# Kernel tuning notes

Hardware: AMD Instinct MI355X
Metric: run time of the kernel (lower is better)

The kernel has to match this reference:

```python
import jax, jax.numpy as jnp
import numpy as np

B, T, F = 2048, 128, 128
H, L, K = 512, 8, 10  # hidden_dim, levels, conv_size
CHUNK = H // L
GATES = 4 * H + 2 * L


def setup_inputs() -> dict:
    key = jax.random.key(0)
    ks = jax.random.split(key, 12)
    s_k = 1.0 / np.sqrt(F + 1)
    s_r = 1.0 / np.sqrt(H + 1)
    s_s = 1.0 / np.sqrt(H)
    s_rs = 1.0 / np.sqrt(H // 6)
    s_c = 1.0 / np.sqrt(H * K)
    return {
        'x': jax.random.normal(ks[0], (B, T, F), jnp.float32),
        'time': jax.random.uniform(ks[1], (B, T), jnp.float32),
        'Wk': jax.random.normal(ks[2], (F + 1, GATES), jnp.float32) * s_k,
        'bk': jnp.zeros((GATES,), jnp.float32),
        'Wr': jax.random.normal(ks[3], (H + 1, GATES), jnp.float32) * s_r,
        'br': jnp.zeros((GATES,), jnp.float32),
        'Ws': jax.random.normal(ks[4], (H, H // 6), jnp.float32) * s_s,
        'bs': jax.random.normal(ks[5], (H // 6,), jnp.float32) * 0.01,
        'Wrs': jax.random.normal(ks[6], (H // 6, H), jnp.float32) * s_rs,
        'brs': jax.random.normal(ks[7], (H,), jnp.float32) * 0.01,
        'conv_w': jax.random.normal(ks[8], (H, H, K), jnp.float32) * s_c,  # [out_ch, in_ch, k]
        'conv_b': jax.random.normal(ks[9], (H,), jnp.float32) * 0.01,
    }


def _cumax_l2r(z):
    return jnp.cumsum(jax.nn.softmax(z, axis=-1), axis=-1)


def _cumax_r2l(z):
    return jnp.flip(jnp.cumsum(jax.nn.softmax(jnp.flip(z, -1), axis=-1), axis=-1), -1)


def _phase_forward(x, time, Wk, bk, Wr, br, Ws, bs, Wrs, brs, conv_w, conv_b):
    def step(carry, xs):
        c, h, tmp_h, tmp_dis = carry
        xt, dt = xs
        dt = dt[:, None]
        xo = (jnp.concatenate([xt, dt], -1) @ Wk + bk
              + jnp.concatenate([h, dt], -1) @ Wr + br)  # [B, 4H+2L]
        fm = _cumax_l2r(xo[:, :L])[:, :, None]        # [B, L, 1]
        im = _cumax_r2l(xo[:, L:2 * L])[:, :, None]   # [B, L, 1]
        g = xo[:, 2 * L:].reshape(-1, 4 * L, CHUNK)
        f = jax.nn.sigmoid(g[:, :L])
        i = jax.nn.sigmoid(g[:, L:2 * L])
        o = jax.nn.sigmoid(g[:, 2 * L:3 * L])
        c_in = jnp.tanh(g[:, 3 * L:])
        c_last = c.reshape(-1, L, CHUNK)
        ov = fm * im
        c_new = ov * (f * c_last + i * c_in) + (fm - ov) * c_last + (im - ov) * c_in
        h_new = (o * jnp.tanh(c_new)).reshape(-1, H)
        dist = 1.0 - jnp.mean(fm[..., 0], axis=-1)   # [B]
        tmp_h = jnp.concatenate([tmp_h[1:], h_new[None]], 0)
        tmp_dis = jnp.concatenate([tmp_dis[1:], dist[None]], 0)
        return (c_new.reshape(-1, H), h_new, tmp_h, tmp_dis), dist

    init = (jnp.zeros((B, H), x.dtype), jnp.zeros((B, H), x.dtype),
            jnp.zeros((K, B, H), x.dtype), jnp.zeros((K, B), x.dtype))
    (_, _, tmp_h, tmp_dis), distance = jax.lax.scan(
        step, init, (jnp.transpose(x, (1, 0, 2)), time.T))

    local_dis = jax.nn.softmax(jnp.cumsum(tmp_dis.T, axis=1), axis=1)   # [B, K]
    local_h = jnp.transpose(tmp_h, (1, 2, 0)) * local_dis[:, None, :]   # [B, H, K]
    theme = jax.nn.sigmoid(
        jnp.maximum(jnp.mean(local_h, axis=-1) @ Ws + bs, 0.0) @ Wrs + brs)  # [B, H]
    conv_out = jnp.einsum('bhk,ohk->bo', local_h, conv_w) + conv_b      # valid conv, out len 1
    return theme * conv_out, distance


def reference(x, time, Wk, bk, Wr, br, Ws, bs, Wrs, brs, conv_w, conv_b):
    return _phase_forward(x, time, Wk, bk, Wr, br, Ws, bs, Wrs, brs, conv_w, conv_b)
```

## Files before the change

### kernel.cpp

```cpp
#include <hip/hip_runtime.h>
#include <hip/hip_bf16.h>
#include <cstddef>
#include <cstdint>

namespace {

constexpr int B = 2048, T = 128, F = 128, H = 512, L = 8, KW = 10;
constexpr int GATES = 2064;
constexpr int NG = 2048;
constexpr int KIN = 640;
constexpr int HS = 85;
constexpr int RC = H * KW;
constexpr int KS = 8;
constexpr int NROW = 144;

typedef __attribute__((ext_vector_type(8))) short short8;
typedef __attribute__((ext_vector_type(4))) float f32x4;
typedef unsigned long long ull;

__device__ __forceinline__ float fsigmoid_(float x) {
    return __builtin_amdgcn_rcpf(1.0f + __expf(-x));
}
__device__ __forceinline__ float ftanh_(float x) {
    return 1.0f - 2.0f * __builtin_amdgcn_rcpf(1.0f + __expf(2.0f * x));
}

__device__ __forceinline__ void gl_lds16(const void* g, void* l) {
    __builtin_amdgcn_global_load_lds(
        (const __attribute__((address_space(1))) unsigned int*)g,
        (__attribute__((address_space(3))) unsigned int*)l,
        16, 0, 0);
}

__device__ __forceinline__ ull h_atomic_load(const void* p) {
    return __hip_atomic_load((const ull*)p, __ATOMIC_RELAXED, __HIP_MEMORY_SCOPE_AGENT);
}

__global__ __launch_bounds__(256) void prep_wgt(
    const float* __restrict__ Wk, const float* __restrict__ Wr,
    __hip_bfloat16* __restrict__ WgT)
{
    __shared__ float tile[64 * 65];
    const int tid = threadIdx.x;
    const int c0 = blockIdx.x * 64, k0 = blockIdx.y * 64;
#pragma unroll
    for (int rep = 0; rep < 16; ++rep) {
        int e = rep * 256 + tid;
        int kl = e >> 6, cl = e & 63;
        int col = c0 + cl;
        int nt = col >> 7, cc = col & 127;
        int n = 16 + ((cc >> 4) & 3) * 512 + nt * 32 + ((cc >> 6) & 1) * 16 + (cc & 15);
        int k = k0 + kl;
        tile[kl * 65 + cl] = (k < F) ? Wk[(size_t)k * GATES + n] : Wr[(size_t)(k - F) * GATES + n];
    }
    __syncthreads();
    const int cl = tid >> 2, q = tid & 3;
    unsigned short buf[16];
#pragma unroll
    for (int i = 0; i < 16; ++i) {
        float f = tile[(q * 16 + i) * 65 + cl];
        __hip_bfloat16 bv = __float2bfloat16(f);
        buf[i] = *(unsigned short*)&bv;
    }
    int col = c0 + cl;
    int nt = col >> 7, rin = col & 127;
    unsigned short* dst = (unsigned short*)WgT + (size_t)nt * NROW * KIN + (size_t)rin * KIN + k0 + q * 16;
    *(short8*)dst = *(short8*)&buf[0];
    *(short8*)(dst + 8) = *(short8*)&buf[8];
}

__global__ void prep_w16rep(const float* __restrict__ Wk, const float* __restrict__ Wr,
                            __hip_bfloat16* __restrict__ WgT)
{
    int idx = blockIdx.x * blockDim.x + threadIdx.x;
    if (idx >= 16 * 16 * KIN) return;
    int nt = idx / (16 * KIN);
    int rem = idx % (16 * KIN);
    int n = rem / KIN, k = rem % KIN;
    float v = (k < F) ? Wk[(size_t)k * GATES + n] : Wr[(size_t)(k - F) * GATES + n];
    WgT[(size_t)nt * NROW * KIN + (size_t)(128 + n) * KIN + k] = __float2bfloat16(v);
}

__global__ void prep_small(const float* __restrict__ Wk, const float* __restrict__ bk,
                           const float* __restrict__ Wr, const float* __restrict__ br,
                           float* __restrict__ biasg, float* __restrict__ wrowg,
                           float* __restrict__ bias16, float* __restrict__ wrow16)
{
    const int total = 2 * NG + 32;
    for (int idx = threadIdx.x; idx < total; idx += 256) {
        if (idx < NG) {
            int col = idx;
            int nt = col >> 7, cc = col & 127;
            int n = 16 + ((cc >> 4) & 3) * 512 + nt * 32 + ((cc >> 6) & 1) * 16 + (cc & 15);
            biasg[col] = bk[n] + br[n];
        } else if (idx < 2 * NG) {
            int col = idx - NG;
            int nt = col >> 7, cc = col & 127;
            int n = 16 + ((cc >> 4) & 3) * 512 + nt * 32 + ((cc >> 6) & 1) * 16 + (cc & 15);
            wrowg[col] = Wk[(size_t)F * GATES + n] + Wr[(size_t)H * GATES + n];
        } else if (idx < 2 * NG + 16) {
            int n = idx - 2 * NG;
            bias16[n] = bk[n] + br[n];
        } else {
            int n = idx - 2 * NG - 16;
            wrow16[n] = Wk[(size_t)F * GATES + n] + Wr[(size_t)H * GATES + n];
        }
    }
}

__global__ void convert_x(const float* __restrict__ x, __hip_bfloat16* __restrict__ xb) {
    int i = blockIdx.x * blockDim.x + threadIdx.x;
    size_t o = (size_t)i * 4;
    if (o >= (size_t)B * T * F) return;
    float4 v = *(const float4*)(x + o);
    xb[o + 0] = __float2bfloat16(v.x);
    xb[o + 1] = __float2bfloat16(v.y);
    xb[o + 2] = __float2bfloat16(v.z);
    xb[o + 3] = __float2bfloat16(v.w);
}

__global__ void prep_convw(const float* __restrict__ conv_w, __hip_bfloat16* __restrict__ CWb) {
    int i = blockIdx.x * blockDim.x + threadIdx.x;
    if (i >= H * RC / 4) return;
    size_t o = (size_t)i * 4;
    float4 v = *(const float4*)(conv_w + o);
    CWb[o + 0] = __float2bfloat16(v.x);
    CWb[o + 1] = __float2bfloat16(v.y);
    CWb[o + 2] = __float2bfloat16(v.z);
    CWb[o + 3] = __float2bfloat16(v.w);
}

struct StepArgs {
    const __hip_bfloat16* xb;
    __hip_bfloat16* h0;
    __hip_bfloat16* h1;
    const __hip_bfloat16* WgT;
    const float* biasg;
    const float* wrowg;
    const float* bias16;
    const float* wrow16;
    const float* tme;
    __hip_bfloat16* tmp_h;
    float* tmp_ds;
    float* dist_out;
    unsigned* bar;
};

__global__ __launch_bounds__(512, 2) void persistent_step(StepArgs a)
{
    __shared__ __align__(16) char smem[34816];
    float* logitS = (float*)smem;
    float* fmimS = (float*)(smem + 8704);
    unsigned short* hstageS = (unsigned short*)(smem + 16896);
    float* dts = (float*)(smem + 25088);

    const int tid = threadIdx.x;
    const int wave = tid >> 6;
    const int wr = wave >> 1, wc = wave & 1;
    const int quad = (tid & 63) >> 4, m16 = tid & 15;
    const int l = blockIdx.x;
    const int nt = ((l & 7) << 1) | ((l >> 3) & 1);
    const int mt = l >> 4;
    const int m0 = mt * 128;

    const int o0 = tid * 16;
    const int arow = o0 >> 6;
    const int asl = ((((o0 >> 4) & 3) ^ ((arow >> 1) & 3)) << 3);
    const char* xbT = (const char*)a.xb + (size_t)(m0 + arow) * (T * F * 2) + asl * 2;
    const size_t hbyte = (size_t)(m0 + arow) * (H * 2) + asl * 2;
    const unsigned short* wgt_tile = (const unsigned short*)a.WgT + (size_t)nt * NROW * KIN;
    const int brow0 = o0 >> 6;
    const int bsl0 = ((((o0 >> 4) & 3) ^ ((brow0 >> 1) & 3)) << 3);
    const char* bsT0 = (const char*)(wgt_tile + (size_t)brow0 * KIN + bsl0);
    const int ob1 = 8192 + tid * 16;
    const int brow1 = ob1 >> 6;
    const int bsl1 = ((((ob1 >> 4) & 3) ^ ((brow1 >> 1) & 3)) << 3);
    const char* bsT1 = (const char*)(wgt_tile + (size_t)brow1 * KIN + bsl1);
    const bool bv1 = (tid < 64);

    const int hcol = nt * 32 + wc * 16 + m16;
    const int lidx = hcol >> 6;
    float bj[4], wj[4];
#pragma unroll
    for (int j = 0; j < 4; ++j) {
        int col = nt * 128 + wc * 64 + j * 16 + m16;
        bj[j] = a.biasg[col];
        wj[j] = a.wrowg[col];
    }
    float b16r[16], w16r[16];
#pragma unroll
    for (int n = 0; n < 16; ++n) { b16r[n] = a.bias16[n]; w16r[n] = a.wrow16[n]; }

    const unsigned short* Abase = (const unsigned short*)smem;
    const unsigned short* Bbase = (const unsigned short*)(smem + 16384);

    float creg[2][4] = {};
    ull areg[2][2];

    {
        gl_lds16(xbT, smem + o0);
        gl_lds16(bsT0, smem + 16384 + o0);
        if (bv1) gl_lds16(bsT1, smem + 16384 + ob1);
        areg[1][0] = *(const ull*)(xbT + 64);  areg[1][1] = *(const ull*)(xbT + 72);
        areg[0][0] = *(const ull*)(xbT + 128); areg[0][1] = *(const ull*)(xbT + 136);
    }
    __syncthreads();

#pragma unroll 1
    for (int t = 0; t < T; ++t) {
        const char* xt = xbT + (size_t)t * 256;
        const char* hs = (const char*)((t & 1) ? a.h1 : a.h0) + hbyte;
        unsigned* hout32 = (unsigned*)((t & 1) ? a.h0 : a.h1);

        f32x4 acc[2][4] = {};
        f32x4 acc16[2] = {};

#pragma unroll
        for (int ki = 0; ki < 20; ++ki) {
            if (ki > 0) {
                if (ki == 1)
                    asm volatile("s_waitcnt vmcnt(1) lgkmcnt(0)" ::: "memory");
                else if (ki <= 17)
                    asm volatile("s_waitcnt vmcnt(2) lgkmcnt(0)" ::: "memory");
                else
                    asm volatile("s_waitcnt vmcnt(0) lgkmcnt(0)" ::: "memory");
                __builtin_amdgcn_s_barrier();
                __builtin_amdgcn_sched_barrier(0);
            }
            const int nxt = ki + 1;
            if (nxt < 20) {
                char* adst = smem + (nxt & 1) * 8192 + o0;
                *(ull*)adst = areg[nxt & 1][0];
                *(ull*)(adst + 8) = areg[nxt & 1][1];
                char* bdst = smem + 16384 + (nxt & 1) * 9216;
                gl_lds16(bsT0 + nxt * 64, bdst + o0);
                if (bv1) gl_lds16(bsT1 + nxt * 64, bdst + ob1);
                __builtin_amdgcn_sched_barrier(0);
                const int fut = ki + 3;
                if (fut < 20) {
                    if (fut <= 3) {
                        areg[fut & 1][0] = *(const ull*)(xt + fut * 64);
                        areg[fut & 1][1] = *(const ull*)(xt + fut * 64 + 8);
                    } else {
                        areg[fut & 1][0] = h_atomic_load(hs + fut * 64 - 256);
                        areg[fut & 1][1] = h_atomic_load(hs + fut * 64 - 248);
                    }
                }
            }
            const unsigned short* A = Abase + (ki & 1) * 4096;
            const unsigned short* Bb = Bbase + (ki & 1) * 4608;
            short8 av[2], bv[4];
#pragma unroll
            for (int i = 0; i < 2; ++i) {
                int ar = wr * 32 + i * 16 + m16;
                av[i] = *(const short8*)&A[ar * 32 + ((quad ^ ((ar >> 1) & 3)) << 3)];
            }
#pragma unroll
            for (int j = 0; j < 4; ++j) {
                int br = wc * 64 + j * 16 + m16;
                bv[j] = *(const short8*)&Bb[br * 32 + ((quad ^ ((br >> 1) & 3)) << 3)];
            }
#pragma unroll
            for (int i = 0; i < 2; ++i)
#pragma unroll
                for (int j = 0; j < 4; ++j)
                    acc[i][j] = __builtin_amdgcn_mfma_f32_16x16x32_bf16(av[i], bv[j], acc[i][j], 0, 0, 0);
            if (wc == 0) {
                int lr = 128 + m16;
                short8 wv = *(const short8*)&Bb[lr * 32 + ((quad ^ ((lr >> 1) & 3)) << 3)];
                acc16[0] = __builtin_amdgcn_mfma_f32_16x16x32_bf16(av[0], wv, acc16[0], 0, 0, 0);
                acc16[1] = __builtin_amdgcn_mfma_f32_16x16x32_bf16(av[1], wv, acc16[1], 0, 0, 0);
            }
        }
        __syncthreads();

        if (wc == 0) {
#pragma unroll
            for (int i = 0; i < 2; ++i)
#pragma unroll
                for (int r = 0; r < 4; ++r)
                    logitS[(wr * 32 + i * 16 + quad * 4 + r) * 17 + m16] = acc16[i][r];
        }
        __syncthreads();

        if (tid < 256) {
            const int row = tid & 127;
            const int m = m0 + row;
            const bool hi = tid >= 128;
            const float dt = a.tme[(size_t)m * T + t];
            if (!hi) dts[row] = dt;
            const int off = hi ? 8 : 0;
            float z[8];
#pragma unroll
            for (int n = 0; n < 8; ++n)
                z[n] = logitS[row * 17 + off + n] + b16r[off + n] + dt * w16r[off + n];
            float mx = z[0];
#pragma unroll
            for (int j = 1; j < 8; ++j) mx = fmaxf(mx, z[j]);
            float e[8], s = 0.f;
#pragma unroll
            for (int j = 0; j < 8; ++j) { e[j] = __expf(z[j] - mx); s += e[j]; }
            if (!hi) {
                float run = 0.f, fsum = 0.f;
#pragma unroll
                for (int j = 0; j < 8; ++j) { run += e[j]; float fmv = run / s; fmimS[row * 16 + j] = fmv; fsum += fmv; }
                if (nt == 0) {
                    float d = 1.0f - fsum * 0.125f;
                    a.dist_out[(size_t)t * B + m] = d;
                    if (t >= T - KW) a.tmp_ds[(size_t)(t - (T - KW)) * B + m] = d;
                }
            } else {
                float run = 0.f;
#pragma unroll
                for (int j = 7; j >= 0; --j) { run += e[j]; fmimS[row * 16 + 8 + j] = run / s; }
            }
        }
        __syncthreads();

#pragma unroll
        for (int i = 0; i < 2; ++i) {
#pragma unroll
            for (int r = 0; r < 4; ++r) {
                int rl = wr * 32 + i * 16 + quad * 4 + r;
                int m = m0 + rl;
                float dt = dts[rl];
                float fmv = fmimS[rl * 16 + lidx];
                float imv = fmimS[rl * 16 + 8 + lidx];
                float fg = fsigmoid_(acc[i][0][r] + bj[0] + dt * wj[0]);
                float ig = fsigmoid_(acc[i][1][r] + bj[1] + dt * wj[1]);
                float og = fsigmoid_(acc[i][2][r] + bj[2] + dt * wj[2]);
                float ci = ftanh_(acc[i][3][r] + bj[3] + dt * wj[3]);
                float ov = fmv * imv;
                float cl = creg[i][r];
                float cn = ov * (fg * cl + ig * ci) + (fmv - ov) * cl + (imv - ov) * ci;
                float hn = og * ftanh_(cn);
                creg[i][r] = cn;
                __hip_bfloat16 hb = __float2bfloat16(hn);
                hstageS[rl * 32 + (wc * 16 + m16)] = *(unsigned short*)&hb;
                if (t >= T - KW) a.tmp_h[((size_t)(t - (T - KW)) * B + m) * H + hcol] = hb;
            }
        }
        __syncthreads();

        {
            const unsigned* hs32 = (const unsigned*)hstageS;
#pragma unroll
            for (int wds = 0; wds < 4; ++wds) {
                int wi = wds * 512 + tid;
                int row = wi >> 4, cp = wi & 15;
                unsigned v = hs32[row * 16 + cp];
                __hip_atomic_store(hout32 + (size_t)(m0 + row) * (H / 2) + nt * 16 + cp, v,
                                   __ATOMIC_RELAXED, __HIP_MEMORY_SCOPE_AGENT);
            }
        }

        __syncthreads();
        if (t != T - 1) {
            const char* xn = xbT + (size_t)(t + 1) * 256;
            gl_lds16(xn, smem + o0);
            gl_lds16(bsT0, smem + 16384 + o0);
            if (bv1) gl_lds16(bsT1, smem + 16384 + ob1);
            areg[1][0] = *(const ull*)(xn + 64);  areg[1][1] = *(const ull*)(xn + 72);
            areg[0][0] = *(const ull*)(xn + 128); areg[0][1] = *(const ull*)(xn + 136);
            if (tid == 0) {
                unsigned* ctr = a.bar + (mt << 6);
                __hip_atomic_fetch_add(ctr, 1u, __ATOMIC_RELAXED, __HIP_MEMORY_SCOPE_AGENT);
                const unsigned tgt = 16u * (unsigned)(t + 1);
                for (int it = 0; it < (1 << 22); ++it) {
                    if (__hip_atomic_load(ctr, __ATOMIC_RELAXED, __HIP_MEMORY_SCOPE_AGENT) >= tgt) break;
                    __builtin_amdgcn_s_sleep(2);
                }
            }
            __syncthreads();
        }
    }
}

__global__ __launch_bounds__(128) void post_local(
    const __hip_bfloat16* __restrict__ tmp_h, const float* __restrict__ tmp_dis,
    float* __restrict__ mean_h, __hip_bfloat16* __restrict__ Ahk)
{
    const int b = blockIdx.x;
    const int tid = threadIdx.x;
    __shared__ float ld[KW];
    if (tid == 0) {
        float cd[KW];
        float run = 0.f;
        for (int k = 0; k < KW; ++k) { run += tmp_dis[(size_t)k * B + b]; cd[k] = run; }
        float mx = cd[0];
        for (int k = 1; k < KW; ++k) mx = fmaxf(mx, cd[k]);
        float s = 0.f;
        for (int k = 0; k < KW; ++k) { cd[k] = expf(cd[k] - mx); s += cd[k]; }
        for (int k = 0; k < KW; ++k) ld[k] = cd[k] / s;
    }
    __syncthreads();
    float ldr[KW];
#pragma unroll
    for (int k = 0; k < KW; ++k) ldr[k] = ld[k];
    for (int h = tid; h < H; h += 128) {
        float s = 0.f;
#pragma unroll
        for (int k = 0; k < KW; ++k) {
            float v = __bfloat162float(tmp_h[((size_t)k * B + b) * H + h]) * ldr[k];
            s += v;
            Ahk[(size_t)b * RC + h * KW + k] = __float2bfloat16(v);
        }
        mean_h[(size_t)b * H + h] = s * (1.0f / KW);
    }
}

__global__ void theme1_k(const float* __restrict__ mean_h, const float* __restrict__ Ws,
                         const float* __restrict__ bs, float* __restrict__ t1)
{
    int idx = blockIdx.x * blockDim.x + threadIdx.x;
    if (idx >= B * HS) return;
    int b = idx / HS, j = idx % HS;
    float s = bs[j];
    const float* mh = mean_h + (size_t)b * H;
    for (int h = 0; h < H; ++h) s += mh[h] * Ws[(size_t)h * HS + j];
    t1[idx] = fmaxf(s, 0.f);
}

__global__ void theme2_k(const float* __restrict__ t1, const float* __restrict__ Wrs,
                         const float* __restrict__ brs, float* __restrict__ theme)
{
    int idx = blockIdx.x * blockDim.x + threadIdx.x;
    if (idx >= B * H) return;
    int b = idx / H, o = idx % H;
    float s = brs[o];
    const float* tv = t1 + (size_t)b * HS;
    for (int j = 0; j < HS; ++j) s += tv[j] * Wrs[(size_t)j * H + o];
    theme[idx] = 1.0f / (1.0f + expf(-s));
}

__global__ __launch_bounds__(256) void conv_split(
    const __hip_bfloat16* __restrict__ Ahk, const __hip_bfloat16* __restrict__ CWb,
    float* __restrict__ Pbuf)
{
    __shared__ __align__(16) unsigned short As2[128 * 64];
    __shared__ __align__(16) unsigned short Bs2[128 * 64];
    const int tid = threadIdx.x;
    const int wave = tid >> 6;
    const int wr = wave >> 1, wc = wave & 1;
    const int quad = (tid & 63) >> 4, m16 = tid & 15;
    const int n0 = blockIdx.x * 128, m0 = blockIdx.y * 128;
    const int ksb = blockIdx.z * (RC / KS);

    f32x4 acc[4][4] = {};
    for (int k0 = 0; k0 < RC / KS; k0 += 64) {
#pragma unroll
        for (int p = 0; p < 4; ++p) {
            int o = p * 4096 + tid * 16;
            int row = o >> 7, slot = (o >> 4) & 7;
            int kg = ksb + k0 + (slot ^ (row & 7)) * 8;
            gl_lds16((const unsigned short*)Ahk + (size_t)(m0 + row) * RC + kg, (char*)As2 + o);
            gl_lds16((const unsigned short*)CWb + (size_t)(n0 + row) * RC + kg, (char*)Bs2 + o);
        }
        __syncthreads();
#pragma unroll
        for (int c2 = 0; c2 < 2; ++c2) {
            const int k8 = c2 * 4 + quad;
            short8 av[4], bv[4];
#pragma unroll
            for (int i = 0; i < 4; ++i) {
                int arow = wr * 64 + i * 16 + m16;
                av[i] = *(const short8*)&As2[arow * 64 + (k8 ^ (arow & 7)) * 8];
            }
#pragma unroll
            for (int j = 0; j < 4; ++j) {
                int brow = wc * 64 + j * 16 + m16;
                bv[j] = *(const short8*)&Bs2[brow * 64 + (k8 ^ (brow & 7)) * 8];
            }
#pragma unroll
            for (int i = 0; i < 4; ++i)
#pragma unroll
                for (int j = 0; j < 4; ++j)
                    acc[i][j] = __builtin_amdgcn_mfma_f32_16x16x32_bf16(av[i], bv[j], acc[i][j], 0, 0, 0);
        }
        __syncthreads();
    }
    float* P = Pbuf + (size_t)blockIdx.z * B * H;
#pragma unroll
    for (int j = 0; j < 4; ++j) {
        const int col = n0 + wc * 64 + j * 16 + m16;
#pragma unroll
        for (int i = 0; i < 4; ++i) {
            const int rb = m0 + wr * 64 + i * 16 + quad * 4;
#pragma unroll
            for (int r = 0; r < 4; ++r)
                P[(size_t)(rb + r) * H + col] = acc[i][j][r];
        }
    }
}

__global__ void conv_reduce(const float* __restrict__ Pbuf, const float* __restrict__ conv_b,
                            const float* __restrict__ theme, float* __restrict__ out0)
{
    int i = blockIdx.x * blockDim.x + threadIdx.x;
    if (i >= B * H) return;
    float s = conv_b[i & (H - 1)];
#pragma unroll
    for (int ks = 0; ks < KS; ++ks) s += Pbuf[(size_t)ks * B * H + i];
    out0[i] = theme[i] * s;
}

}

extern "C" void kernel_launch(void* const* d_in, const int* in_sizes, int n_in,
                              void* d_out, int out_size, void* d_ws, size_t ws_size,
                              hipStream_t stream)
{
    (void)in_sizes; (void)n_in; (void)out_size; (void)ws_size;
    const float* x      = (const float*)d_in[0];
    const float* tme    = (const float*)d_in[1];
    const float* Wk     = (const float*)d_in[2];
    const float* bk     = (const float*)d_in[3];
    const float* Wr     = (const float*)d_in[4];
    const float* br     = (const float*)d_in[5];
    const float* Ws     = (const float*)d_in[6];
    const float* bs     = (const float*)d_in[7];
    const float* Wrs    = (const float*)d_in[8];
    const float* brs    = (const float*)d_in[9];
    const float* conv_w = (const float*)d_in[10];
    const float* conv_b = (const float*)d_in[11];

    float* out0 = (float*)d_out;
    float* dist_out = out0 + (size_t)B * H;

    char* w = (char*)d_ws;
    __hip_bfloat16* WgT  = (__hip_bfloat16*)w; w += (size_t)16 * NROW * KIN * 2;
    __hip_bfloat16* xb   = (__hip_bfloat16*)w; w += (size_t)B * T * F * 2;
    __hip_bfloat16* CWb  = (__hip_bfloat16*)w; w += (size_t)H * RC * 2;
    __hip_bfloat16* Ahk  = (__hip_bfloat16*)w; w += (size_t)B * RC * 2;
    __hip_bfloat16* hb0  = (__hip_bfloat16*)w; w += (size_t)B * H * 2;
    __hip_bfloat16* hb1  = (__hip_bfloat16*)w; w += (size_t)B * H * 2;
    __hip_bfloat16* tmp_h = (__hip_bfloat16*)w; w += (size_t)KW * B * H * 2;
    float* biasg  = (float*)w; w += (size_t)NG * 4;
    float* wrowg  = (float*)w; w += (size_t)NG * 4;
    float* bias16 = (float*)w; w += 64;
    float* wrow16 = (float*)w; w += 64;
    float* tmp_ds = (float*)w; w += (size_t)KW * B * 4;
    float* mean_h = (float*)w; w += (size_t)B * H * 4;
    float* t1     = (float*)w; w += (size_t)B * HS * 4;
    float* theme  = (float*)w; w += (size_t)B * H * 4;
    float* Pbuf   = (float*)w; w += (size_t)KS * B * H * 4;
    unsigned* bar = (unsigned*)w; w += 4096;

    hipMemsetAsync(hb0, 0, (size_t)B * H * sizeof(__hip_bfloat16), stream);
    hipMemsetAsync(bar, 0, 4096, stream);

    prep_wgt<<<dim3(NG / 64, KIN / 64), 256, 0, stream>>>(Wk, Wr, WgT);
    prep_w16rep<<<(16 * 16 * KIN + 255) / 256, 256, 0, stream>>>(Wk, Wr, WgT);
    prep_small<<<1, 256, 0, stream>>>(Wk, bk, Wr, br, biasg, wrowg, bias16, wrow16);
    convert_x<<<((B * T * F / 4) + 255) / 256, 256, 0, stream>>>(x, xb);
    prep_convw<<<((H * RC / 4) + 255) / 256, 256, 0, stream>>>(conv_w, CWb);

    {
        StepArgs sa;
        sa.xb = xb; sa.h0 = hb0; sa.h1 = hb1; sa.WgT = WgT;
        sa.biasg = biasg; sa.wrowg = wrowg; sa.bias16 = bias16; sa.wrow16 = wrow16;
        sa.tme = tme; sa.tmp_h = tmp_h; sa.tmp_ds = tmp_ds; sa.dist_out = dist_out;
        sa.bar = bar;
        persistent_step<<<256, 512, 0, stream>>>(sa);
    }

    post_local<<<B, 128, 0, stream>>>(tmp_h, tmp_ds, mean_h, Ahk);
    theme1_k<<<(B * HS + 255) / 256, 256, 0, stream>>>(mean_h, Ws, bs, t1);
    theme2_k<<<(B * H + 255) / 256, 256, 0, stream>>>(t1, Wrs, brs, theme);
    conv_split<<<dim3(H / 128, B / 128, KS), 256, 0, stream>>>(Ahk, CWb, Pbuf);
    conv_reduce<<<(B * H + 255) / 256, 256, 0, stream>>>(Pbuf, conv_b, theme, out0);
}
```

Measured before the change: 2.099 ms.

## Keep most of weight tile resident in LDS across timesteps, rotate remainder

The persistent recurrent kernel now preloads 12 of the 20 K-slices of its weight tile into shared memory once and keeps them resident for all timesteps. The remaining slices stream through a 3-slot rotating buffer, so per-step global weight traffic drops to a fraction of what it was. LDS grows from about 34KB to about 155KB, so only one 512-thread block fits per CU (launch_bounds still asks for 2), which lowers occupancy. Time values are pre-transposed so each step reads them coalesced into LDS, and the softmax divisions become a single reciprocal multiply.

```diff
diff --git a/kernel.cpp b/kernel.cpp
--- a/kernel.cpp
+++ b/kernel.cpp
@@ -13,6 +13,12 @@
 constexpr int RC = H * KW;
 constexpr int KS = 8;
 constexpr int NROW = 144;
+
+constexpr int ABUF = 0;
+constexpr int BRES = 16384;
+constexpr int BROT = 126976;
+constexpr int DTSO = 154624;
+constexpr int SMEM_SZ = 155136;
 
 typedef __attribute__((ext_vector_type(8))) short short8;
 typedef __attribute__((ext_vector_type(4))) float f32x4;
@@ -130,6 +136,21 @@
     CWb[o + 3] = __float2bfloat16(v.w);
 }
 
+__global__ __launch_bounds__(256) void prep_tmet(const float* __restrict__ tin,
+                                                 float* __restrict__ tout)
+{
+    __shared__ float tl[32][33];
+    const int bb = blockIdx.x * 32, tt = blockIdx.y * 32;
+    const int tx = threadIdx.x & 31, ty = threadIdx.x >> 5;
+#pragma unroll
+    for (int r = 0; r < 32; r += 8)
+        tl[ty + r][tx] = tin[(size_t)(bb + ty + r) * T + tt + tx];
+    __syncthreads();
+#pragma unroll
+    for (int r = 0; r < 32; r += 8)
+        tout[(size_t)(tt + ty + r) * B + bb + tx] = tl[tx][ty + r];
+}
+
 struct StepArgs {
     const __hip_bfloat16* xb;
     __hip_bfloat16* h0;
@@ -139,7 +160,7 @@
     const float* wrowg;
     const float* bias16;
     const float* wrow16;
-    const float* tme;
+    const float* tmeT;
     __hip_bfloat16* tmp_h;
     float* tmp_ds;
     float* dist_out;
@@ -148,11 +169,11 @@
 
 __global__ __launch_bounds__(512, 2) void persistent_step(StepArgs a)
 {
-    __shared__ __align__(16) char smem[34816];
+    __shared__ __align__(16) char smem[SMEM_SZ];
     float* logitS = (float*)smem;
-    float* fmimS = (float*)(smem + 8704);
-    unsigned short* hstageS = (unsigned short*)(smem + 16896);
-    float* dts = (float*)(smem + 25088);
+    float* fmimS = (float*)(smem + BROT);
+    unsigned short* hstageS = (unsigned short*)(smem + 135168);
+    float* dts = (float*)(smem + DTSO);
 
     const int tid = threadIdx.x;
     const int wave = tid >> 6;
@@ -178,6 +199,11 @@
     const char* bsT1 = (const char*)(wgt_tile + (size_t)brow1 * KIN + bsl1);
     const bool bv1 = (tid < 64);
 
+    auto stageB = [&](int s, int bufbyte) {
+        gl_lds16(bsT0 + s * 64, smem + bufbyte + o0);
+        if (bv1) gl_lds16(bsT1 + s * 64, smem + bufbyte + ob1);
+    };
+
     const int hcol = nt * 32 + wc * 16 + m16;
     const int lidx = hcol >> 6;
     float bj[4], wj[4];
@@ -192,17 +218,18 @@
     for (int n = 0; n < 16; ++n) { b16r[n] = a.bias16[n]; w16r[n] = a.wrow16[n]; }
 
     const unsigned short* Abase = (const unsigned short*)smem;
-    const unsigned short* Bbase = (const unsigned short*)(smem + 16384);
 
     float creg[2][4] = {};
     ull areg[2][2];
 
     {
+#pragma unroll
+        for (int s = 0; s < 12; ++s) stageB(s, BRES + s * 9216);
         gl_lds16(xbT, smem + o0);
-        gl_lds16(bsT0, smem + 16384 + o0);
-        if (bv1) gl_lds16(bsT1, smem + 16384 + ob1);
-        areg[1][0] = *(const ull*)(xbT + 64);  areg[1][1] = *(const ull*)(xbT + 72);
-        areg[0][0] = *(const ull*)(xbT + 128); areg[0][1] = *(const ull*)(xbT + 136);
+        stageB(12, BROT + 0 * 9216);
+        stageB(13, BROT + 1 * 9216);
+        areg[1][0] = h_atomic_load(xbT + 64);  areg[1][1] = h_atomic_load(xbT + 72);
+        areg[0][0] = h_atomic_load(xbT + 128); areg[0][1] = h_atomic_load(xbT + 136);
     }
     __syncthreads();
 
@@ -212,18 +239,25 @@
         const char* hs = (const char*)((t & 1) ? a.h1 : a.h0) + hbyte;
         unsigned* hout32 = (unsigned*)((t & 1) ? a.h0 : a.h1);
 
+        if (tid < 128) dts[tid] = a.tmeT[(size_t)t * B + m0 + tid];
+
         f32x4 acc[2][4] = {};
         f32x4 acc16[2] = {};
 
 #pragma unroll
         for (int ki = 0; ki < 20; ++ki) {
             if (ki > 0) {
-                if (ki == 1)
-                    asm volatile("s_waitcnt vmcnt(1) lgkmcnt(0)" ::: "memory");
-                else if (ki <= 17)
-                    asm volatile("s_waitcnt vmcnt(2) lgkmcnt(0)" ::: "memory");
-                else
+                if (ki <= 13) {
+                    asm volatile("s_waitcnt lgkmcnt(0)" ::: "memory");
+                } else if (ki <= 17) {
+                    if (bv1) asm volatile("s_waitcnt vmcnt(6) lgkmcnt(0)" ::: "memory");
+                    else     asm volatile("s_waitcnt vmcnt(5) lgkmcnt(0)" ::: "memory");
+                } else if (ki == 18) {
+                    if (bv1) asm volatile("s_waitcnt vmcnt(4) lgkmcnt(0)" ::: "memory");
+                    else     asm volatile("s_waitcnt vmcnt(3) lgkmcnt(0)" ::: "memory");
+                } else {
                     asm volatile("s_waitcnt vmcnt(0) lgkmcnt(0)" ::: "memory");
+                }
                 __builtin_amdgcn_s_barrier();
                 __builtin_amdgcn_sched_barrier(0);
             }
@@ -232,23 +266,26 @@
                 char* adst = smem + (nxt & 1) * 8192 + o0;
                 *(ull*)adst = areg[nxt & 1][0];
                 *(ull*)(adst + 8) = areg[nxt & 1][1];
-                char* bdst = smem + 16384 + (nxt & 1) * 9216;
-                gl_lds16(bsT0 + nxt * 64, bdst + o0);
-                if (bv1) gl_lds16(bsT1 + nxt * 64, bdst + ob1);
-                __builtin_amdgcn_sched_barrier(0);
-                const int fut = ki + 3;
-                if (fut < 20) {
-                    if (fut <= 3) {
-                        areg[fut & 1][0] = *(const ull*)(xt + fut * 64);
-                        areg[fut & 1][1] = *(const ull*)(xt + fut * 64 + 8);
-                    } else {
-                        areg[fut & 1][0] = h_atomic_load(hs + fut * 64 - 256);
-                        areg[fut & 1][1] = h_atomic_load(hs + fut * 64 - 248);
-                    }
+            }
+            if (ki >= 12 && ki <= 17) {
+                const int s = ki + 2;
+                stageB(s, BROT + ((s - 12) % 3) * 9216);
+            }
+            __builtin_amdgcn_sched_barrier(0);
+            const int fut = ki + 3;
+            if (fut < 20) {
+                if (fut <= 3) {
+                    areg[fut & 1][0] = h_atomic_load(xt + fut * 64);
+                    areg[fut & 1][1] = h_atomic_load(xt + fut * 64 + 8);
+                } else {
+                    areg[fut & 1][0] = h_atomic_load(hs + fut * 64 - 256);
+                    areg[fut & 1][1] = h_atomic_load(hs + fut * 64 - 248);
                 }
             }
+            __builtin_amdgcn_sched_barrier(0);
             const unsigned short* A = Abase + (ki & 1) * 4096;
-            const unsigned short* Bb = Bbase + (ki & 1) * 4608;
+            const unsigned short* Bb = (const unsigned short*)
+                (smem + (ki < 12 ? BRES + ki * 9216 : BROT + ((ki - 12) % 3) * 9216));
             short8 av[2], bv[4];
 #pragma unroll
             for (int i = 0; i < 2; ++i) {
@@ -287,8 +324,7 @@
             const int row = tid & 127;
             const int m = m0 + row;
             const bool hi = tid >= 128;
-            const float dt = a.tme[(size_t)m * T + t];
-            if (!hi) dts[row] = dt;
+            const float dt = dts[row];
             const int off = hi ? 8 : 0;
             float z[8];
 #pragma unroll
@@ -300,10 +336,11 @@
             float e[8], s = 0.f;
 #pragma unroll
             for (int j = 0; j < 8; ++j) { e[j] = __expf(z[j] - mx); s += e[j]; }
+            const float inv = __builtin_amdgcn_rcpf(s);
             if (!hi) {
                 float run = 0.f, fsum = 0.f;
 #pragma unroll
-                for (int j = 0; j < 8; ++j) { run += e[j]; float fmv = run / s; fmimS[row * 16 + j] = fmv; fsum += fmv; }
+                for (int j = 0; j < 8; ++j) { run += e[j]; float fmv = run * inv; fmimS[row * 16 + j] = fmv; fsum += fmv; }
                 if (nt == 0) {
                     float d = 1.0f - fsum * 0.125f;
                     a.dist_out[(size_t)t * B + m] = d;
@@ -312,7 +349,7 @@
             } else {
                 float run = 0.f;
 #pragma unroll
-                for (int j = 7; j >= 0; --j) { run += e[j]; fmimS[row * 16 + 8 + j] = run / s; }
+                for (int j = 7; j >= 0; --j) { run += e[j]; fmimS[row * 16 + 8 + j] = run * inv; }
             }
         }
         __syncthreads();
@@ -358,10 +395,10 @@
         if (t != T - 1) {
             const char* xn = xbT + (size_t)(t + 1) * 256;
             gl_lds16(xn, smem + o0);
-            gl_lds16(bsT0, smem + 16384 + o0);
-            if (bv1) gl_lds16(bsT1, smem + 16384 + ob1);
-            areg[1][0] = *(const ull*)(xn + 64);  areg[1][1] = *(const ull*)(xn + 72);
-            areg[0][0] = *(const ull*)(xn + 128); areg[0][1] = *(const ull*)(xn + 136);
+            stageB(12, BROT + 0 * 9216);
+            stageB(13, BROT + 1 * 9216);
+            areg[1][0] = h_atomic_load(xn + 64);  areg[1][1] = h_atomic_load(xn + 72);
+            areg[0][0] = h_atomic_load(xn + 128); areg[0][1] = h_atomic_load(xn + 136);
             if (tid == 0) {
                 unsigned* ctr = a.bar + (mt << 6);
                 __hip_atomic_fetch_add(ctr, 1u, __ATOMIC_RELAXED, __HIP_MEMORY_SCOPE_AGENT);
@@ -544,6 +581,7 @@
     float* t1     = (float*)w; w += (size_t)B * HS * 4;
     float* theme  = (float*)w; w += (size_t)B * H * 4;
     float* Pbuf   = (float*)w; w += (size_t)KS * B * H * 4;
+    float* tmeT   = (float*)w; w += (size_t)T * B * 4;
     unsigned* bar = (unsigned*)w; w += 4096;
 
     hipMemsetAsync(hb0, 0, (size_t)B * H * sizeof(__hip_bfloat16), stream);
@@ -554,12 +592,13 @@
     prep_small<<<1, 256, 0, stream>>>(Wk, bk, Wr, br, biasg, wrowg, bias16, wrow16);
     convert_x<<<((B * T * F / 4) + 255) / 256, 256, 0, stream>>>(x, xb);
     prep_convw<<<((H * RC / 4) + 255) / 256, 256, 0, stream>>>(conv_w, CWb);
+    prep_tmet<<<dim3(B / 32, T / 32), 256, 0, stream>>>(tme, tmeT);
 
     {
         StepArgs sa;
         sa.xb = xb; sa.h0 = hb0; sa.h1 = hb1; sa.WgT = WgT;
         sa.biasg = biasg; sa.wrowg = wrowg; sa.bias16 = bias16; sa.wrow16 = wrow16;
-        sa.tme = tme; sa.tmp_h = tmp_h; sa.tmp_ds = tmp_ds; sa.dist_out = dist_out;
+        sa.tmeT = tmeT; sa.tmp_h = tmp_h; sa.tmp_ds = tmp_ds; sa.dist_out = dist_out;
         sa.bar = bar;
         persistent_step<<<256, 512, 0, stream>>>(sa);
     }
```

Measured after the change: 1.771 ms. 1.19x faster.
